# Kernel tuning notes

Measured on AMD Instinct MI355X. Metric: run time of the kernel, lower is better.

The kernel has to match this reference:

```python
import jax, jax.numpy as jnp
import numpy as np

B, L, H, V = 256, 2048, 64, 64


def setup_inputs() -> dict:
    key = jax.random.key(0)
    ks = jax.random.split(key, 16)
    s = 0.05
    return {
        "seq": jax.random.randint(ks[0], (B, L), 0, V),
        "embed": jax.random.normal(ks[1], (V, H), jnp.float32) * s,
        "W1": jax.random.normal(ks[2], (2 * H, H), jnp.float32) * s,
        "b1": jnp.zeros((2 * H,), jnp.float32),
        "W2": jax.random.normal(ks[3], (H, 2 * H), jnp.float32) * s,
        "b2": jnp.zeros((H,), jnp.float32),
        "gamma": jnp.ones((H,), jnp.float32),
        "beta": jnp.zeros((H,), jnp.float32),
        "Wk": jax.random.normal(ks[4], (H, H), jnp.float32) * s,
        "Wv": jax.random.normal(ks[5], (H, H), jnp.float32) * s,
        "Wq": jax.random.normal(ks[6], (H, H), jnp.float32) * s,
        "Wrp": jax.random.normal(ks[7], (H, H), jnp.float32) * s,
        "brp": jnp.zeros((H,), jnp.float32),
        "Wout": jax.random.normal(ks[8], (V, H), jnp.float32) * s,
        "bout": jnp.zeros((V,), jnp.float32),
    }


def reference(seq, embed, W1, b1, W2, b2, gamma, beta, Wk, Wv, Wq, Wrp, brp, Wout, bout):
    # encode: LayerNorm(e + FF(e))
    e = embed[seq]                                   # [B, L, H]
    ff = jnp.maximum(e @ W1.T + b1, 0.0) @ W2.T + b2  # [B, L, H]
    h = e + ff
    mu = h.mean(-1, keepdims=True)
    var = ((h - mu) ** 2).mean(-1, keepdims=True)    # torch LN: biased var, eps=1e-5
    hs = (h - mu) / jnp.sqrt(var + 1e-5) * gamma + beta

    # precompute k/v for the first L-1 steps (batched GEMM)
    k_all = hs[:, :-1] @ Wk.T                         # [B, L-1, H]
    v_all = hs[:, :-1] @ Wv.T                         # [B, L-1, H]
    # F.normalize(k, dim=-1): k / max(||k||, 1e-12)
    k_n = k_all / jnp.maximum(jnp.linalg.norm(k_all, axis=-1, keepdims=True), 1e-12)

    def step(M, kv):
        k, v = kv                                      # each [B, H]
        vp = jnp.einsum('bij,bj->bi', M, k)
        M = M + jnp.einsum('bi,bj->bij', v - vp, k)    # rank-1 delta update
        return M, None

    M0 = jnp.zeros((B, H, H), hs.dtype)
    M, _ = jax.lax.scan(step, M0, (jnp.swapaxes(k_n, 0, 1), jnp.swapaxes(v_all, 0, 1)))

    q = hs[:, -1] @ Wq.T                               # [B, H]
    r = jnp.einsum('bij,bj->bi', M, q) @ Wrp.T + brp
    return r @ Wout.T + bout                           # [B, V]
```

## Files before the change

kernel.cpp:

```cpp
#include <hip/hip_runtime.h>


#define DPP_ADD_F32(x, ctrl, rm, bm, bc)                                      \
  (x) = (x) + __int_as_float(__builtin_amdgcn_update_dpp(                     \
            0, __float_as_int(x), (ctrl), (rm), (bm), (bc)))

__device__ __forceinline__ float wave_sum64(float x) {
  DPP_ADD_F32(x, 0x111, 0xf, 0xf, true);
  DPP_ADD_F32(x, 0x112, 0xf, 0xf, true);
  DPP_ADD_F32(x, 0x114, 0xf, 0xf, true);
  DPP_ADD_F32(x, 0x118, 0xf, 0xf, true);
  DPP_ADD_F32(x, 0x142, 0xa, 0xf, false);
  DPP_ADD_F32(x, 0x143, 0xc, 0xf, false);
  return __int_as_float(__builtin_amdgcn_readlane(__float_as_int(x), 63));
}

__device__ __forceinline__ float readlane_f(float x, int lane) {
  return __int_as_float(__builtin_amdgcn_readlane(__float_as_int(x), lane));
}

__global__ __launch_bounds__(64) void build_tables(
    const float* __restrict__ embed, const float* __restrict__ W1,
    const float* __restrict__ b1, const float* __restrict__ W2,
    const float* __restrict__ b2, const float* __restrict__ gamma,
    const float* __restrict__ beta, const float* __restrict__ Wk,
    const float* __restrict__ Wv, const float* __restrict__ Wq,
    float* __restrict__ k_tab, float* __restrict__ v_tab,
    float* __restrict__ q_tab) {
  __shared__ float Wbuf[8448];
  __shared__ float e_s[64];
  __shared__ float f1_s[128];
  __shared__ float hs_s[64];
  const int tok = blockIdx.x;
  const int l = threadIdx.x;

  const float e = embed[tok * 64 + l];
  e_s[l] = e;
  for (int i = 0; i < 128; ++i) Wbuf[i * 65 + l] = W1[i * 64 + l];
  __syncthreads();

  float a0 = b1[l], a1 = b1[l + 64];
#pragma unroll
  for (int h = 0; h < 64; ++h) {
    a0 = fmaf(e_s[h], Wbuf[l * 65 + h], a0);
    a1 = fmaf(e_s[h], Wbuf[(l + 64) * 65 + h], a1);
  }
  f1_s[l] = fmaxf(a0, 0.f);
  f1_s[l + 64] = fmaxf(a1, 0.f);
  __syncthreads();

  for (int i = 0; i < 128; ++i)
    Wbuf[(i >> 1) * 131 + (i & 1) * 64 + l] = W2[i * 64 + l];
  __syncthreads();

  float acc = b2[l];
#pragma unroll
  for (int j = 0; j < 128; ++j) acc = fmaf(f1_s[j], Wbuf[l * 131 + j], acc);
  const float hval = e + acc;

  const float mu = wave_sum64(hval) * (1.f / 64.f);
  const float d = hval - mu;
  const float var = wave_sum64(d * d) * (1.f / 64.f);
  const float hs = d * (1.f / sqrtf(var + 1e-5f)) * gamma[l] + beta[l];
  hs_s[l] = hs;
  __syncthreads();

  for (int i = 0; i < 64; ++i) {
    Wbuf[i * 65 + l] = Wk[i * 64 + l];
    Wbuf[4224 + i * 65 + l] = Wv[i * 64 + l];
  }
  __syncthreads();
  float kk = 0.f, vv = 0.f;
#pragma unroll
  for (int h = 0; h < 64; ++h) {
    kk = fmaf(hs_s[h], Wbuf[l * 65 + h], kk);
    vv = fmaf(hs_s[h], Wbuf[4224 + l * 65 + h], vv);
  }
  __syncthreads();
  for (int i = 0; i < 64; ++i) Wbuf[i * 65 + l] = Wq[i * 64 + l];
  __syncthreads();
  float qq = 0.f;
#pragma unroll
  for (int h = 0; h < 64; ++h) qq = fmaf(hs_s[h], Wbuf[l * 65 + h], qq);

  float nrm = fmaxf(sqrtf(wave_sum64(kk * kk)), 1e-12f);
  k_tab[tok * 64 + l] = kk / nrm;
  v_tab[tok * 64 + l] = vv;
  q_tab[tok * 64 + l] = qq;
}

__global__ __launch_bounds__(64) void build_gram(
    const float* __restrict__ k_tab, const float* __restrict__ q_tab,
    const float* __restrict__ v_tab, float2* __restrict__ GV,
    float* __restrict__ KQ) {
  __shared__ float k_s[4160];
  __shared__ float q_s[64];
  const int a = blockIdx.x;
  const int l = threadIdx.x;
  for (int i = 0; i < 64; ++i) k_s[i * 65 + l] = k_tab[i * 64 + l];
  q_s[l] = q_tab[a * 64 + l];
  __syncthreads();
  float g = 0.f, kq = 0.f;
#pragma unroll
  for (int h = 0; h < 64; ++h) {
    g = fmaf(k_s[a * 65 + h], k_s[l * 65 + h], g);
    kq = fmaf(q_s[h], k_s[l * 65 + h], kq);
  }
  GV[a * 64 + l] = make_float2(g, v_tab[a * 64 + l]);
  KQ[a * 64 + l] = kq;
}

__global__ __launch_bounds__(64, 1) void scan_head(
    const int* __restrict__ seq, const float2* __restrict__ GVg,
    const float* __restrict__ KQ, const float* __restrict__ Wrp,
    const float* __restrict__ brp, const float* __restrict__ Wout,
    const float* __restrict__ bout, float* __restrict__ out) {
  __shared__ float2 GV_s[4160];
  __shared__ float tmp[64];
  const int b = blockIdx.x;
  const int l = threadIdx.x;

#pragma unroll
  for (int i = 0; i < 32; ++i)
    ((float4*)GV_s)[l + 64 * i] = ((const float4*)GVg)[l + 64 * i];
  GV_s[4096 + l] = make_float2(0.f, 0.f);

  const int* tokp = seq + b * 2048;
  int tok_cur = tokp[2047 - l];
  int tok_nxt = tokp[2047 - 64 - l];
  __syncthreads();

  const int qt = __builtin_amdgcn_readlane(tok_cur, 0);
  float y = KQ[qt * 64 + l];
  float r = 0.f;
  if (l == 0) tok_cur = 64;

  float2 gA[64], gB[64];
#pragma unroll
  for (int j = 0; j < 64; ++j) {
    const int bj = __builtin_amdgcn_readlane(tok_cur, j);
    gA[j] = GV_s[bj * 64 + l];
  }

  for (int n = 0; n < 16; ++n) {
    const int i2 = 2 * n + 2, i3 = 2 * n + 3;
    int tok_f1 = (i2 <= 31) ? tokp[2047 - 64 * i2 - l] : 0;
#pragma unroll
    for (int j = 0; j < 64; ++j) {
      const int bn = __builtin_amdgcn_readlane(tok_nxt, j);
      const float2 gv = GV_s[bn * 64 + l];
      const int bc = __builtin_amdgcn_readlane(tok_cur, j) & 63;
      const float s = readlane_f(y, bc);
      y = fmaf(-s, gA[j].x, y);
      r = fmaf(s, gA[j].y, r);
      gB[j] = gv;
    }
    tok_cur = tok_nxt;
    tok_nxt = tok_f1;
    int tok_f2 = (i3 <= 31) ? tokp[2047 - 64 * i3 - l] : 0;
#pragma unroll
    for (int j = 0; j < 64; ++j) {
      const int bn = __builtin_amdgcn_readlane(tok_nxt, j);
      const float2 gv = GV_s[bn * 64 + l];
      const int bc = __builtin_amdgcn_readlane(tok_cur, j) & 63;
      const float s = readlane_f(y, bc);
      y = fmaf(-s, gB[j].x, y);
      r = fmaf(s, gB[j].y, r);
      gA[j] = gv;
    }
    tok_cur = tok_nxt;
    tok_nxt = tok_f2;
  }

  float* Wb = (float*)GV_s;
  tmp[l] = r;
  for (int i = 0; i < 64; ++i) {
    Wb[i * 65 + l] = Wrp[i * 64 + l];
    Wb[4160 + i * 65 + l] = Wout[i * 64 + l];
  }
  __syncthreads();
  float acc = brp[l];
#pragma unroll
  for (int j = 0; j < 64; ++j) acc = fmaf(tmp[j], Wb[l * 65 + j], acc);
  __syncthreads();
  tmp[l] = acc;
  __syncthreads();
  float o = bout[l];
#pragma unroll
  for (int i = 0; i < 64; ++i) o = fmaf(tmp[i], Wb[4160 + l * 65 + i], o);
  out[b * 64 + l] = o;
}

extern "C" void kernel_launch(void* const* d_in, const int* in_sizes, int n_in,
                              void* d_out, int out_size, void* d_ws,
                              size_t ws_size, hipStream_t stream) {
  const int* seq = (const int*)d_in[0];
  const float* embed = (const float*)d_in[1];
  const float* W1 = (const float*)d_in[2];
  const float* b1 = (const float*)d_in[3];
  const float* W2 = (const float*)d_in[4];
  const float* b2 = (const float*)d_in[5];
  const float* gamma = (const float*)d_in[6];
  const float* beta = (const float*)d_in[7];
  const float* Wk = (const float*)d_in[8];
  const float* Wv = (const float*)d_in[9];
  const float* Wq = (const float*)d_in[10];
  const float* Wrp = (const float*)d_in[11];
  const float* brp = (const float*)d_in[12];
  const float* Wout = (const float*)d_in[13];
  const float* bout = (const float*)d_in[14];

  float* wsf = (float*)d_ws;
  float* k_tab = wsf;
  float* v_tab = wsf + 4096;
  float* q_tab = wsf + 8192;
  float2* GV = (float2*)(wsf + 12288);
  float* KQ = wsf + 20480;

  build_tables<<<64, 64, 0, stream>>>(embed, W1, b1, W2, b2, gamma, beta, Wk,
                                      Wv, Wq, k_tab, v_tab, q_tab);
  build_gram<<<64, 64, 0, stream>>>(k_tab, q_tab, v_tab, GV, KQ);
  scan_head<<<256, 64, 0, stream>>>(seq, GV, KQ, Wrp, brp, Wout, bout,
                                    (float*)d_out);
}
```

Measured before the change: 133.4 us.

## Interleave two batch scans per wave with rolling 8-deep prefetch ring

The scan kernel now processes two batch rows per 64-thread block, interleaving their independent serial dependency chains to hide readlane and FMA latency. The 128-entry double-buffered register arrays are replaced by an 8-slot rolling prefetch ring of LDS loads, which cuts register pressure. The Gram term is negated in build_gram so the inner update becomes a plain FMA. Grid size halves to 128 blocks, so fewer CUs are occupied and each block does twice the serial work.

```diff
diff --git a/kernel.cpp b/kernel.cpp
--- a/kernel.cpp
+++ b/kernel.cpp
@@ -106,89 +106,109 @@
     g = fmaf(k_s[a * 65 + h], k_s[l * 65 + h], g);
     kq = fmaf(q_s[h], k_s[l * 65 + h], kq);
   }
-  GV[a * 64 + l] = make_float2(g, v_tab[a * 64 + l]);
+  GV[a * 64 + l] = make_float2(-g, v_tab[a * 64 + l]);
   KQ[a * 64 + l] = kq;
 }
 
-__global__ __launch_bounds__(64, 1) void scan_head(
+__global__ __launch_bounds__(64, 1) void scan_head2(
     const int* __restrict__ seq, const float2* __restrict__ GVg,
     const float* __restrict__ KQ, const float* __restrict__ Wrp,
     const float* __restrict__ brp, const float* __restrict__ Wout,
     const float* __restrict__ bout, float* __restrict__ out) {
   __shared__ float2 GV_s[4160];
-  __shared__ float tmp[64];
-  const int b = blockIdx.x;
+  __shared__ float tmp[128];
+  const int b0 = blockIdx.x * 2, b1 = b0 + 1;
   const int l = threadIdx.x;
 
 #pragma unroll
   for (int i = 0; i < 32; ++i)
     ((float4*)GV_s)[l + 64 * i] = ((const float4*)GVg)[l + 64 * i];
   GV_s[4096 + l] = make_float2(0.f, 0.f);
-
-  const int* tokp = seq + b * 2048;
-  int tok_cur = tokp[2047 - l];
-  int tok_nxt = tokp[2047 - 64 - l];
-  __syncthreads();
-
-  const int qt = __builtin_amdgcn_readlane(tok_cur, 0);
-  float y = KQ[qt * 64 + l];
-  float r = 0.f;
-  if (l == 0) tok_cur = 64;
-
-  float2 gA[64], gB[64];
-#pragma unroll
-  for (int j = 0; j < 64; ++j) {
-    const int bj = __builtin_amdgcn_readlane(tok_cur, j);
-    gA[j] = GV_s[bj * 64 + l];
-  }
-
-  for (int n = 0; n < 16; ++n) {
-    const int i2 = 2 * n + 2, i3 = 2 * n + 3;
-    int tok_f1 = (i2 <= 31) ? tokp[2047 - 64 * i2 - l] : 0;
+  __syncthreads();
+
+  const int* tp0 = seq + b0 * 2048;
+  const int* tp1 = seq + b1 * 2048;
+  float y0 = KQ[tp0[2047] * 64 + l];
+  float y1 = KQ[tp1[2047] * 64 + l];
+  float r0 = 0.f, r1 = 0.f;
+
+  int tokA0 = (l == 0) ? 64 : tp0[2047 - l];
+  int tokA1 = (l == 0) ? 64 : tp1[2047 - l];
+  int tokB0 = tp0[2047 - 64 - l];
+  int tokB1 = tp1[2047 - 64 - l];
+
+  float2 c0[8], c1[8];
+  int s0[8], s1[8];
+#pragma unroll
+  for (int k = 0; k < 8; ++k) {
+    s0[k] = __builtin_amdgcn_readlane(tokA0, k);
+    c0[k] = GV_s[s0[k] * 64 + l];
+    s1[k] = __builtin_amdgcn_readlane(tokA1, k);
+    c1[k] = GV_s[s1[k] * 64 + l];
+  }
+
+  for (int blk = 0; blk < 32; ++blk) {
+    int nx0 = (blk + 2 < 32) ? tp0[2047 - 64 * (blk + 2) - l] : 64;
+    int nx1 = (blk + 2 < 32) ? tp1[2047 - 64 * (blk + 2) - l] : 64;
 #pragma unroll
     for (int j = 0; j < 64; ++j) {
-      const int bn = __builtin_amdgcn_readlane(tok_nxt, j);
-      const float2 gv = GV_s[bn * 64 + l];
-      const int bc = __builtin_amdgcn_readlane(tok_cur, j) & 63;
-      const float s = readlane_f(y, bc);
-      y = fmaf(-s, gA[j].x, y);
-      r = fmaf(s, gA[j].y, r);
-      gB[j] = gv;
+      const int ip = j + 8;
+      {
+        const float2 gv = c0[j & 7];
+        const int bc = s0[j & 7] & 63;
+        const int sl = (ip < 64) ? __builtin_amdgcn_readlane(tokA0, ip)
+                                 : __builtin_amdgcn_readlane(tokB0, ip - 64);
+        s0[j & 7] = sl;
+        c0[j & 7] = GV_s[sl * 64 + l];
+        const float s = readlane_f(y0, bc);
+        y0 = fmaf(s, gv.x, y0);
+        r0 = fmaf(s, gv.y, r0);
+      }
+      {
+        const float2 gv = c1[j & 7];
+        const int bc = s1[j & 7] & 63;
+        const int sl = (ip < 64) ? __builtin_amdgcn_readlane(tokA1, ip)
+                                 : __builtin_amdgcn_readlane(tokB1, ip - 64);
+        s1[j & 7] = sl;
+        c1[j & 7] = GV_s[sl * 64 + l];
+        const float s = readlane_f(y1, bc);
+        y1 = fmaf(s, gv.x, y1);
+        r1 = fmaf(s, gv.y, r1);
+      }
     }
-    tok_cur = tok_nxt;
-    tok_nxt = tok_f1;
-    int tok_f2 = (i3 <= 31) ? tokp[2047 - 64 * i3 - l] : 0;
-#pragma unroll
-    for (int j = 0; j < 64; ++j) {
-      const int bn = __builtin_amdgcn_readlane(tok_nxt, j);
-      const float2 gv = GV_s[bn * 64 + l];
-      const int bc = __builtin_amdgcn_readlane(tok_cur, j) & 63;
-      const float s = readlane_f(y, bc);
-      y = fmaf(-s, gB[j].x, y);
-      r = fmaf(s, gB[j].y, r);
-      gA[j] = gv;
-    }
-    tok_cur = tok_nxt;
-    tok_nxt = tok_f2;
+    tokA0 = tokB0;
+    tokB0 = nx0;
+    tokA1 = tokB1;
+    tokB1 = nx1;
   }
 
   float* Wb = (float*)GV_s;
-  tmp[l] = r;
+  tmp[l] = r0;
+  tmp[64 + l] = r1;
+  __syncthreads();
   for (int i = 0; i < 64; ++i) {
     Wb[i * 65 + l] = Wrp[i * 64 + l];
     Wb[4160 + i * 65 + l] = Wout[i * 64 + l];
   }
   __syncthreads();
-  float acc = brp[l];
-#pragma unroll
-  for (int j = 0; j < 64; ++j) acc = fmaf(tmp[j], Wb[l * 65 + j], acc);
-  __syncthreads();
-  tmp[l] = acc;
-  __syncthreads();
-  float o = bout[l];
-#pragma unroll
-  for (int i = 0; i < 64; ++i) o = fmaf(tmp[i], Wb[4160 + l * 65 + i], o);
-  out[b * 64 + l] = o;
+  float a0 = brp[l], a1 = brp[l];
+#pragma unroll
+  for (int j = 0; j < 64; ++j) {
+    a0 = fmaf(tmp[j], Wb[l * 65 + j], a0);
+    a1 = fmaf(tmp[64 + j], Wb[l * 65 + j], a1);
+  }
+  __syncthreads();
+  tmp[l] = a0;
+  tmp[64 + l] = a1;
+  __syncthreads();
+  float o0 = bout[l], o1 = bout[l];
+#pragma unroll
+  for (int i = 0; i < 64; ++i) {
+    o0 = fmaf(tmp[i], Wb[4160 + l * 65 + i], o0);
+    o1 = fmaf(tmp[64 + i], Wb[4160 + l * 65 + i], o1);
+  }
+  out[b0 * 64 + l] = o0;
+  out[b1 * 64 + l] = o1;
 }
 
 extern "C" void kernel_launch(void* const* d_in, const int* in_sizes, int n_in,
@@ -220,6 +240,6 @@
   build_tables<<<64, 64, 0, stream>>>(embed, W1, b1, W2, b2, gamma, beta, Wk,
                                       Wv, Wq, k_tab, v_tab, q_tab);
   build_gram<<<64, 64, 0, stream>>>(k_tab, q_tab, v_tab, GV, KQ);
-  scan_head<<<256, 64, 0, stream>>>(seq, GV, KQ, Wrp, brp, Wout, bout,
-                                    (float*)d_out);
-}
+  scan_head2<<<128, 64, 0, stream>>>(seq, GV, KQ, Wrp, brp, Wout, bout,
+                                     (float*)d_out);
+}
```

After: 163.7 us. 22.8% more time.

## Pack reversed tokens into 6-bit words and pipeline scan with scalar indices

Applied to the files above, without the earlier changes.

Adds a pre-pass kernel that packs five reversed 6-bit tokens per int, so the scan reads token indices as uniform scalar values from LDS instead of using per-lane token registers and readlane. The scan is restructured into a 5-stage rotating register pipeline of prefetched GV entries with a shorter lookahead, replacing the 64-wide double buffers. This should cut VGPR pressure and readlane work. The Gram sign is folded into the table so each step uses a plain FMA. It adds an extra kernel launch and a workspace buffer, plus more complex tail handling.

```diff
diff --git a/kernel.cpp b/kernel.cpp
--- a/kernel.cpp
+++ b/kernel.cpp
@@ -106,16 +106,33 @@
     g = fmaf(k_s[a * 65 + h], k_s[l * 65 + h], g);
     kq = fmaf(q_s[h], k_s[l * 65 + h], kq);
   }
-  GV[a * 64 + l] = make_float2(g, v_tab[a * 64 + l]);
+  GV[a * 64 + l] = make_float2(-g, v_tab[a * 64 + l]);
   KQ[a * 64 + l] = kq;
+}
+
+__global__ __launch_bounds__(256) void pack_tokens(const int* __restrict__ seq,
+                                                   int* __restrict__ pk) {
+  const int idx = blockIdx.x * 256 + threadIdx.x;
+  const int b = idx / 410, w = idx - b * 410;
+  const int* tp = seq + b * 2048;
+  int acc = 0;
+#pragma unroll
+  for (int i = 0; i < 5; ++i) {
+    const int j = 5 * w + 1 + i;
+    const int t = (j <= 2047) ? tp[2047 - j] : 0;
+    acc |= t << (6 * i);
+  }
+  pk[b * 412 + w] = acc;
 }
 
 __global__ __launch_bounds__(64, 1) void scan_head(
     const int* __restrict__ seq, const float2* __restrict__ GVg,
-    const float* __restrict__ KQ, const float* __restrict__ Wrp,
-    const float* __restrict__ brp, const float* __restrict__ Wout,
-    const float* __restrict__ bout, float* __restrict__ out) {
+    const float* __restrict__ KQ, const int* __restrict__ pk,
+    const float* __restrict__ Wrp, const float* __restrict__ brp,
+    const float* __restrict__ Wout, const float* __restrict__ bout,
+    float* __restrict__ out) {
   __shared__ float2 GV_s[4160];
+  __shared__ int pk_s[448];
   __shared__ float tmp[64];
   const int b = blockIdx.x;
   const int l = threadIdx.x;
@@ -123,57 +140,84 @@
 #pragma unroll
   for (int i = 0; i < 32; ++i)
     ((float4*)GV_s)[l + 64 * i] = ((const float4*)GVg)[l + 64 * i];
-  GV_s[4096 + l] = make_float2(0.f, 0.f);
+  const int* pkb = pk + b * 412;
+#pragma unroll
+  for (int i = 0; i < 7; ++i) {
+    const int idx = l + 64 * i;
+    pk_s[idx] = (idx < 410) ? pkb[idx] : 0;
+  }
+  __syncthreads();
 
   const int* tokp = seq + b * 2048;
-  int tok_cur = tokp[2047 - l];
-  int tok_nxt = tokp[2047 - 64 - l];
-  __syncthreads();
-
-  const int qt = __builtin_amdgcn_readlane(tok_cur, 0);
+  const int qt = tokp[2047];
   float y = KQ[qt * 64 + l];
   float r = 0.f;
-  if (l == 0) tok_cur = 64;
-
-  float2 gA[64], gB[64];
-#pragma unroll
-  for (int j = 0; j < 64; ++j) {
-    const int bj = __builtin_amdgcn_readlane(tok_cur, j);
-    gA[j] = GV_s[bj * 64 + l];
-  }
-
-  for (int n = 0; n < 16; ++n) {
-    const int i2 = 2 * n + 2, i3 = 2 * n + 3;
-    int tok_f1 = (i2 <= 31) ? tokp[2047 - 64 * i2 - l] : 0;
-#pragma unroll
-    for (int j = 0; j < 64; ++j) {
-      const int bn = __builtin_amdgcn_readlane(tok_nxt, j);
-      const float2 gv = GV_s[bn * 64 + l];
-      const int bc = __builtin_amdgcn_readlane(tok_cur, j) & 63;
-      const float s = readlane_f(y, bc);
-      y = fmaf(-s, gA[j].x, y);
-      r = fmaf(s, gA[j].y, r);
-      gB[j] = gv;
+
+  int S[5][5];
+  int vw[5];
+#pragma unroll
+  for (int k = 0; k < 5; ++k) {
+    const int u = __builtin_amdgcn_readfirstlane(pk_s[k]);
+#pragma unroll
+    for (int i = 0; i < 5; ++i) S[k][i] = (u >> (6 * i)) & 63;
+  }
+  vw[0] = pk_s[5];
+  vw[1] = pk_s[6];
+  vw[2] = 0;
+  vw[3] = 0;
+  vw[4] = 0;
+
+  float2 c[25];
+#pragma unroll
+  for (int s = 0; s < 20; ++s) c[s] = GV_s[S[s / 5][s % 5] * 64 + l];
+
+  for (int m = 0; m < 81; ++m) {
+    const int wb = 5 * m;
+#pragma unroll
+    for (int q = 0; q < 5; ++q) {
+      vw[(q + 2) % 5] = pk_s[wb + q + 7];
+#pragma unroll
+      for (int i = 0; i < 5; ++i) {
+        const float2 gv = c[5 * q + i];
+        c[(q == 0) ? (20 + i) : (5 * q - 5 + i)] =
+            GV_s[S[(q + 4) % 5][i] * 64 + l];
+        const float sv = readlane_f(y, S[q][i]);
+        y = fmaf(sv, gv.x, y);
+        r = fmaf(sv, gv.y, r);
+      }
+      const int u = __builtin_amdgcn_readfirstlane(vw[q]);
+#pragma unroll
+      for (int i = 0; i < 5; ++i) S[q][i] = (u >> (6 * i)) & 63;
     }
-    tok_cur = tok_nxt;
-    tok_nxt = tok_f1;
-    int tok_f2 = (i3 <= 31) ? tokp[2047 - 64 * i3 - l] : 0;
-#pragma unroll
-    for (int j = 0; j < 64; ++j) {
-      const int bn = __builtin_amdgcn_readlane(tok_nxt, j);
-      const float2 gv = GV_s[bn * 64 + l];
-      const int bc = __builtin_amdgcn_readlane(tok_cur, j) & 63;
-      const float s = readlane_f(y, bc);
-      y = fmaf(-s, gB[j].x, y);
-      r = fmaf(s, gB[j].y, r);
-      gA[j] = gv;
+  }
+
+#pragma unroll
+  for (int q = 0; q < 4; ++q) {
+#pragma unroll
+    for (int i = 0; i < 5; ++i) {
+      const float2 gv = c[5 * q + i];
+      c[(q == 0) ? (20 + i) : (5 * q - 5 + i)] =
+          GV_s[S[(q + 4) % 5][i] * 64 + l];
+      const float sv = readlane_f(y, S[q][i]);
+      y = fmaf(sv, gv.x, y);
+      r = fmaf(sv, gv.y, r);
     }
-    tok_cur = tok_nxt;
-    tok_nxt = tok_f2;
+  }
+  {
+    const float2 gv = c[20];
+    const float sv = readlane_f(y, S[4][0]);
+    y = fmaf(sv, gv.x, y);
+    r = fmaf(sv, gv.y, r);
+  }
+  {
+    const float2 gv = c[21];
+    const float sv = readlane_f(y, S[4][1]);
+    r = fmaf(sv, gv.y, r);
   }
 
   float* Wb = (float*)GV_s;
   tmp[l] = r;
+  __syncthreads();
   for (int i = 0; i < 64; ++i) {
     Wb[i * 65 + l] = Wrp[i * 64 + l];
     Wb[4160 + i * 65 + l] = Wout[i * 64 + l];
@@ -216,10 +260,12 @@
   float* q_tab = wsf + 8192;
   float2* GV = (float2*)(wsf + 12288);
   float* KQ = wsf + 20480;
+  int* pk = (int*)(wsf + 24576);
 
   build_tables<<<64, 64, 0, stream>>>(embed, W1, b1, W2, b2, gamma, beta, Wk,
                                       Wv, Wq, k_tab, v_tab, q_tab);
   build_gram<<<64, 64, 0, stream>>>(k_tab, q_tab, v_tab, GV, KQ);
-  scan_head<<<256, 64, 0, stream>>>(seq, GV, KQ, Wrp, brp, Wout, bout,
+  pack_tokens<<<410, 256, 0, stream>>>(seq, pk);
+  scan_head<<<256, 64, 0, stream>>>(seq, GV, KQ, pk, Wrp, brp, Wout, bout,
                                     (float*)d_out);
 }
```

After: 148.3 us. 11.2% more time.

## Pipeline scan recurrence with bpermute lookahead and precomputed Gram coupling terms

Applied to the files above, without the earlier changes.

Rewrites the scan inner loop into a software pipeline. Token indices and y-lane values are fetched with ds_bpermute a few steps ahead instead of readlane, and the dependent scalar is computed as s_j = y_b + G[c_j,c_{j-1}]*s_{j-1}, so each step no longer waits on the previous y update before its cross-lane read. The Gram matrix is stored negated and in a padded 65-stride shared layout with a zero row and column for the dummy token. The aim is to cut the serial readlane latency chain per step, at the cost of extra LDS loads and more complex index bookkeeping.

```diff
diff --git a/kernel.cpp b/kernel.cpp
--- a/kernel.cpp
+++ b/kernel.cpp
@@ -15,8 +15,9 @@
   return __int_as_float(__builtin_amdgcn_readlane(__float_as_int(x), 63));
 }
 
-__device__ __forceinline__ float readlane_f(float x, int lane) {
-  return __int_as_float(__builtin_amdgcn_readlane(__float_as_int(x), lane));
+__device__ __forceinline__ float bperm_f(int byte_addr, float v) {
+  return __int_as_float(
+      __builtin_amdgcn_ds_bpermute(byte_addr, __float_as_int(v)));
 }
 
 __global__ __launch_bounds__(64) void build_tables(
@@ -106,7 +107,7 @@
     g = fmaf(k_s[a * 65 + h], k_s[l * 65 + h], g);
     kq = fmaf(q_s[h], k_s[l * 65 + h], kq);
   }
-  GV[a * 64 + l] = make_float2(g, v_tab[a * 64 + l]);
+  GV[a * 64 + l] = make_float2(-g, v_tab[a * 64 + l]);
   KQ[a * 64 + l] = kq;
 }
 
@@ -115,65 +116,71 @@
     const float* __restrict__ KQ, const float* __restrict__ Wrp,
     const float* __restrict__ brp, const float* __restrict__ Wout,
     const float* __restrict__ bout, float* __restrict__ out) {
-  __shared__ float2 GV_s[4160];
+  __shared__ float2 GV_s[4225];
   __shared__ float tmp[64];
   const int b = blockIdx.x;
   const int l = threadIdx.x;
 
-#pragma unroll
-  for (int i = 0; i < 32; ++i)
-    ((float4*)GV_s)[l + 64 * i] = ((const float4*)GVg)[l + 64 * i];
-  GV_s[4096 + l] = make_float2(0.f, 0.f);
+  for (int t = 0; t < 64; ++t) GV_s[t * 65 + l] = GVg[t * 64 + l];
+  GV_s[64 * 65 + l] = make_float2(0.f, 0.f);
+  GV_s[l * 65 + 64] = make_float2(0.f, 0.f);
+  if (l == 0) GV_s[64 * 65 + 64] = make_float2(0.f, 0.f);
+  __syncthreads();
 
   const int* tokp = seq + b * 2048;
-  int tok_cur = tokp[2047 - l];
-  int tok_nxt = tokp[2047 - 64 - l];
-  __syncthreads();
-
-  const int qt = __builtin_amdgcn_readlane(tok_cur, 0);
+  const int qt = tokp[2047];
   float y = KQ[qt * 64 + l];
   float r = 0.f;
-  if (l == 0) tok_cur = 64;
-
-  float2 gA[64], gB[64];
-#pragma unroll
-  for (int j = 0; j < 64; ++j) {
-    const int bj = __builtin_amdgcn_readlane(tok_cur, j);
-    gA[j] = GV_s[bj * 64 + l];
-  }
-
-  for (int n = 0; n < 16; ++n) {
-    const int i2 = 2 * n + 2, i3 = 2 * n + 3;
-    int tok_f1 = (i2 <= 31) ? tokp[2047 - 64 * i2 - l] : 0;
+
+  int tok_cur = (l == 0) ? 64 : tokp[2047 - l];
+  int tok_nxt = tokp[2047 - 64 - l];
+
+  int cbR[8];
+  int t65R[4];
+  float2 colR[4];
+  float cfR[4];
+  float ybR[4];
+
+#pragma unroll
+  for (int t = 0; t < 8; ++t)
+    cbR[t] = __builtin_amdgcn_ds_bpermute(4 * t, tok_cur);
+#pragma unroll
+  for (int t = 0; t < 4; ++t) colR[t] = GV_s[cbR[t] * 65 + l];
+  t65R[2] = cbR[2] * 65;
+  t65R[3] = cbR[3] * 65;
+  cfR[0] = 0.f;
+  cfR[1] = GV_s[cbR[1] * 65 + cbR[0]].x;
+  ybR[0] = bperm_f((cbR[0] & 63) << 2, y);
+  ybR[1] = bperm_f((cbR[1] & 63) << 2, y);
+  float s_prev = 0.f;
+  int idxv = 32;
+
+  for (int blk = 0; blk < 32; ++blk) {
+    const int tok_fut =
+        (blk + 2 < 32) ? tokp[2047 - 64 * (blk + 2) - l] : 64;
 #pragma unroll
     for (int j = 0; j < 64; ++j) {
-      const int bn = __builtin_amdgcn_readlane(tok_nxt, j);
-      const float2 gv = GV_s[bn * 64 + l];
-      const int bc = __builtin_amdgcn_readlane(tok_cur, j) & 63;
-      const float s = readlane_f(y, bc);
-      y = fmaf(-s, gA[j].x, y);
-      r = fmaf(s, gA[j].y, r);
-      gB[j] = gv;
+      cbR[j & 7] =
+          __builtin_amdgcn_ds_bpermute(idxv, (j < 56) ? tok_cur : tok_nxt);
+      idxv = (j == 55) ? 0 : idxv + 4;
+      const float2 gv = colR[j & 3];
+      const int t65 = cbR[(j + 4) & 7] * 65;
+      t65R[(j + 4) & 3] = t65;
+      colR[j & 3] = GV_s[t65 + l];
+      cfR[(j + 2) & 3] = GV_s[t65R[(j + 2) & 3] + cbR[(j + 1) & 7]].x;
+      const float sj = fmaf(cfR[j & 3], s_prev, ybR[j & 3]);
+      y = fmaf(sj, gv.x, y);
+      r = fmaf(sj, gv.y, r);
+      ybR[(j + 2) & 3] = bperm_f((cbR[(j + 2) & 7] & 63) << 2, y);
+      s_prev = sj;
     }
     tok_cur = tok_nxt;
-    tok_nxt = tok_f1;
-    int tok_f2 = (i3 <= 31) ? tokp[2047 - 64 * i3 - l] : 0;
-#pragma unroll
-    for (int j = 0; j < 64; ++j) {
-      const int bn = __builtin_amdgcn_readlane(tok_nxt, j);
-      const float2 gv = GV_s[bn * 64 + l];
-      const int bc = __builtin_amdgcn_readlane(tok_cur, j) & 63;
-      const float s = readlane_f(y, bc);
-      y = fmaf(-s, gB[j].x, y);
-      r = fmaf(s, gB[j].y, r);
-      gA[j] = gv;
-    }
-    tok_cur = tok_nxt;
-    tok_nxt = tok_f2;
+    tok_nxt = tok_fut;
   }
 
   float* Wb = (float*)GV_s;
   tmp[l] = r;
+  __syncthreads();
   for (int i = 0; i < 64; ++i) {
     Wb[i * 65 + l] = Wrp[i * 64 + l];
     Wb[4160 + i * 65 + l] = Wout[i * 64 + l];
```

Measured after the change: 170.2 us. 27.6% more time.
